# Optimization experiments

Measured on AMD Instinct MI355X. Metric: run time of the kernel, lower is better.

## Reference

```python
import jax, jax.numpy as jnp
import numpy as np

MAX_BLUR = 20.0
MIN_BLUR = 0.5
MIN_SCALE = 0.001


def _dct_matrix(N, dtype):
    """Orthonormal DCT-II matrix C: dct(v) = C @ v (matches torch_dct norm='ortho')."""
    n = jnp.arange(N, dtype=dtype)
    k = n[:, None]
    C = jnp.cos(jnp.pi * (n[None, :] + 0.5) * k / N)
    scale = jnp.where(k == 0, jnp.sqrt(jnp.asarray(1.0 / N, dtype)), jnp.sqrt(jnp.asarray(2.0 / N, dtype)))
    return C * scale


def setup_inputs() -> dict:
    key = jax.random.key(0)
    k1, k2 = jax.random.split(key)
    x = jax.random.normal(k1, (128, 3, 256, 256), dtype=jnp.float32)
    t = jax.random.uniform(k2, (128,), dtype=jnp.float32)
    return {"x": x, "t": t}


def reference(x, t):
    dtype = x.dtype
    N = x.shape[-1]
    # frequency grid: pi * linspace(0, N-1, N) / N, squared and summed over 2D
    freqs = jnp.pi * jnp.arange(N, dtype=dtype) / N
    freq_sq = freqs[:, None] ** 2 + freqs[None, :] ** 2  # [N, N]

    # blur schedule: exp(log(min_blur)*(1-t) + log(max_blur)*t)
    sigmas = jnp.exp(np.log(MIN_BLUR) * (1.0 - t) + np.log(MAX_BLUR) * t)
    sigmas = sigmas[:, None, None, None]  # [B,1,1,1]
    tau = sigmas ** 2 / 2

    fade_freq = jnp.exp(-freq_sq * tau)  # [B,1,N,N]
    fade_freq = jnp.where(fade_freq < 0.01, jnp.zeros((), dtype), fade_freq)

    C = _dct_matrix(N, dtype)  # [N, N]
    # separable 2D DCT-II (ortho): out[k,n] = sum_{h,w} C[k,h] C[n,w] x[h,w]
    dct_x = jnp.einsum('kh,nw,bchw->bckn', C, C, x)
    blurred_dct = dct_x * (fade_freq * (1.0 - MIN_SCALE) + MIN_SCALE)
    # inverse 2D DCT (ortho): transpose matrices
    blurred_x = jnp.einsum('kh,nw,bckn->bchw', C, C, blurred_dct)
    return blurred_x.astype(dtype)
```

## Files before the change

### kernel.cpp

```cpp
#include <hip/hip_runtime.h>
#include <hip/hip_fp16.h>

typedef _Float16 f16;
typedef _Float16 f16x8 __attribute__((ext_vector_type(8)));
typedef _Float16 f16x4 __attribute__((ext_vector_type(4)));
typedef float f32x16 __attribute__((ext_vector_type(16)));

#define NSZ 256
#define NIMG 384

__device__ __forceinline__ int sw(int r, int c) {
  return r * NSZ + (c ^ ((r & 15) << 3));
}

__device__ __forceinline__ int frag_off(int r, int c) {
  return (((((r >> 5) * 16 + (c >> 4)) << 6) + (((c >> 3) & 1) << 5) + (r & 31)) << 3) + (c & 7);
}

__global__ void prep_kernel(f16* __restrict__ Cf, f16* __restrict__ CTf,
                            float* __restrict__ g, const float* __restrict__ t) {
  int k = blockIdx.x;
  int h = threadIdx.x;
  double scale = (k == 0) ? 0.0625 : 0.08838834764831844;
  double val = cos(3.14159265358979323846 * ((double)h + 0.5) * (double)k / 256.0) * scale;
  f16 vh = (f16)((float)val);
  Cf[frag_off(k, h)] = vh;
  CTf[frag_off(h, k)] = vh;
  if (k < 128) {
    float tb = t[k];
    float sg = expf(-0.69314718055994531f * (1.0f - tb) + 2.99573227355399099f * tb);
    float tau = 0.5f * sg * sg;
    float f = 3.14159265358979f * (float)h / 256.0f;
    g[k * NSZ + h] = expf(-f * f * tau);
  }
}

#define TBL_FRAG(Tf, tile, q, lane) (*(const f16x8*)&(Tf)[((((tile) * 16 + (q)) << 6) + (lane)) << 3])

__device__ __forceinline__ void gemm_AL_BT(const f16* L, const f16* __restrict__ Tf,
                                           int rbase, int tB0, int lane,
                                           f32x16 (&acc)[4][2]) {
  int l31 = lane & 31, kh = (lane >> 5) * 8;
#pragma unroll 4
  for (int q = 0; q < 16; ++q) {
    f16x8 a[4], b[2];
#pragma unroll
    for (int fi = 0; fi < 4; ++fi)
      a[fi] = *(const f16x8*)&L[sw(rbase + fi * 32 + l31, q * 16 + kh)];
#pragma unroll
    for (int fj = 0; fj < 2; ++fj)
      b[fj] = TBL_FRAG(Tf, tB0 + fj, q, lane);
#pragma unroll
    for (int fi = 0; fi < 4; ++fi)
#pragma unroll
      for (int fj = 0; fj < 2; ++fj)
        acc[fi][fj] = __builtin_amdgcn_mfma_f32_32x32x16_f16(a[fi], b[fj], acc[fi][fj], 0, 0, 0);
  }
}

__device__ __forceinline__ void writeT(f16* L, int rbase, int cbase, int lane,
                                       const f32x16 (&acc)[4][2]) {
  int l31 = lane & 31, hi4 = (lane >> 5) * 4;
#pragma unroll
  for (int fi = 0; fi < 4; ++fi)
#pragma unroll
    for (int fj = 0; fj < 2; ++fj) {
      int crow = cbase + fj * 32 + l31;
#pragma unroll
      for (int v2 = 0; v2 < 4; ++v2) {
        int colbase = rbase + fi * 32 + v2 * 8 + hi4;
        f16x4 hv;
        hv[0] = (f16)acc[fi][fj][v2 * 4 + 0];
        hv[1] = (f16)acc[fi][fj][v2 * 4 + 1];
        hv[2] = (f16)acc[fi][fj][v2 * 4 + 2];
        hv[3] = (f16)acc[fi][fj][v2 * 4 + 3];
        *(f16x4*)&L[sw(crow, colbase)] = hv;
      }
    }
}

__global__ __launch_bounds__(512, 2) void fused_kernel(
    const float* __restrict__ x, float* __restrict__ out,
    const f16* __restrict__ Cf, const f16* __restrict__ CTf,
    const float* __restrict__ g) {
  __shared__ f16 L[NSZ * NSZ];

  const int img = blockIdx.x;
  const int b = img / 3;
  const float* X = x + (size_t)img * 65536;
  float* Y = out + (size_t)img * 65536;

  const int t = threadIdx.x;
  const int lane = t & 63;
  const int wave = t >> 6;
  const int r0 = (wave >> 2) * 128;
  const int c0 = (wave & 3) * 64;
  const int l31 = lane & 31;
  const int kh = (lane >> 5) * 8;
  const int hi4 = (lane >> 5) * 4;
  const int tB0 = c0 >> 5;

  f32x16 acc[4][2];
  const f32x16 zz = {0.f, 0.f, 0.f, 0.f, 0.f, 0.f, 0.f, 0.f,
                     0.f, 0.f, 0.f, 0.f, 0.f, 0.f, 0.f, 0.f};
#pragma unroll
  for (int fi = 0; fi < 4; ++fi)
#pragma unroll
    for (int fj = 0; fj < 2; ++fj) acc[fi][fj] = zz;

  const int xr_row = t >> 1;
  const int xr_half = (t & 1) * 32;
  float4 xa[2][8];
#pragma unroll
  for (int s = 0; s < 8; ++s) xa[0][s] = *(const float4*)&X[xr_row * NSZ + xr_half + s * 4];

#pragma unroll
  for (int cw = 0; cw < 4; ++cw) {
    int cb = cw & 1;
    if (cw < 3) {
#pragma unroll
      for (int s = 0; s < 8; ++s)
        xa[cb ^ 1][s] = *(const float4*)&X[xr_row * NSZ + (cw + 1) * 64 + xr_half + s * 4];
    }
#pragma unroll
    for (int g8 = 0; g8 < 4; ++g8) {
      float4 a0 = xa[cb][g8 * 2], a1 = xa[cb][g8 * 2 + 1];
      f16x8 v;
      v[0] = (f16)a0.x; v[1] = (f16)a0.y; v[2] = (f16)a0.z; v[3] = (f16)a0.w;
      v[4] = (f16)a1.x; v[5] = (f16)a1.y; v[6] = (f16)a1.z; v[7] = (f16)a1.w;
      *(f16x8*)&L[sw(xr_row, cw * 64 + xr_half + g8 * 8)] = v;
    }
    __syncthreads();
#pragma unroll
    for (int q4 = 0; q4 < 4; ++q4) {
      int q = cw * 4 + q4;
      f16x8 a[4], bfr[2];
#pragma unroll
      for (int fi = 0; fi < 4; ++fi)
        a[fi] = *(const f16x8*)&L[sw(r0 + fi * 32 + l31, q * 16 + kh)];
#pragma unroll
      for (int fj = 0; fj < 2; ++fj)
        bfr[fj] = TBL_FRAG(Cf, tB0 + fj, q, lane);
#pragma unroll
      for (int fi = 0; fi < 4; ++fi)
#pragma unroll
        for (int fj = 0; fj < 2; ++fj)
          acc[fi][fj] = __builtin_amdgcn_mfma_f32_32x32x16_f16(a[fi], bfr[fj], acc[fi][fj], 0, 0, 0);
    }
    __syncthreads();
  }
  writeT(L, r0, c0, lane, acc);
  __syncthreads();

#pragma unroll
  for (int fi = 0; fi < 4; ++fi)
#pragma unroll
    for (int fj = 0; fj < 2; ++fj) acc[fi][fj] = zz;
  gemm_AL_BT(L, Cf, r0, tB0, lane, acc);
  {
    const float* gb = g + b * NSZ;
#pragma unroll
    for (int fj = 0; fj < 2; ++fj) {
      float gk = gb[c0 + fj * 32 + l31];
#pragma unroll
      for (int fi = 0; fi < 4; ++fi) {
#pragma unroll
        for (int v2 = 0; v2 < 4; ++v2) {
          float4 gn = *(const float4*)&gb[r0 + fi * 32 + v2 * 8 + hi4];
          float gnv[4] = {gn.x, gn.y, gn.z, gn.w};
#pragma unroll
          for (int e = 0; e < 4; ++e) {
            float fade = gk * gnv[e];
            float s = ((fade < 0.01f) ? 0.f : fade) * 0.999f + 0.001f;
            acc[fi][fj][v2 * 4 + e] *= s;
          }
        }
      }
    }
  }
  __syncthreads();
  writeT(L, r0, c0, lane, acc);
  __syncthreads();

#pragma unroll
  for (int fi = 0; fi < 4; ++fi)
#pragma unroll
    for (int fj = 0; fj < 2; ++fj) acc[fi][fj] = zz;
  gemm_AL_BT(L, CTf, r0, tB0, lane, acc);
  __syncthreads();
  writeT(L, r0, c0, lane, acc);
  __syncthreads();

#pragma unroll
  for (int fi = 0; fi < 4; ++fi)
#pragma unroll
    for (int fj = 0; fj < 2; ++fj) acc[fi][fj] = zz;
  {
    int tA0 = r0 >> 5;
#pragma unroll 4
    for (int q = 0; q < 16; ++q) {
      f16x8 a[4], bfr[2];
#pragma unroll
      for (int fi = 0; fi < 4; ++fi)
        a[fi] = TBL_FRAG(CTf, tA0 + fi, q, lane);
#pragma unroll
      for (int fj = 0; fj < 2; ++fj)
        bfr[fj] = *(const f16x8*)&L[sw(c0 + fj * 32 + l31, q * 16 + kh)];
#pragma unroll
      for (int fi = 0; fi < 4; ++fi)
#pragma unroll
        for (int fj = 0; fj < 2; ++fj)
          acc[fi][fj] = __builtin_amdgcn_mfma_f32_32x32x16_f16(a[fi], bfr[fj], acc[fi][fj], 0, 0, 0);
    }
  }
#pragma unroll
  for (int fi = 0; fi < 4; ++fi)
#pragma unroll
    for (int fj = 0; fj < 2; ++fj) {
      int w = c0 + fj * 32 + l31;
#pragma unroll
      for (int v2 = 0; v2 < 4; ++v2) {
#pragma unroll
        for (int e = 0; e < 4; ++e) {
          int h = r0 + fi * 32 + v2 * 8 + hi4 + e;
          Y[h * NSZ + w] = acc[fi][fj][v2 * 4 + e];
        }
      }
    }
}

extern "C" void kernel_launch(void* const* d_in, const int* in_sizes, int n_in,
                              void* d_out, int out_size, void* d_ws, size_t ws_size,
                              hipStream_t stream) {
  const float* x = (const float*)d_in[0];
  const float* t = (const float*)d_in[1];
  float* out = (float*)d_out;

  char* ws = (char*)d_ws;
  float* g = (float*)ws;
  f16* Cf = (f16*)(ws + 131072);
  f16* CTf = (f16*)(ws + 262144);

  prep_kernel<<<256, 256, 0, stream>>>(Cf, CTf, g, t);
  fused_kernel<<<NIMG, 512, 0, stream>>>(x, out, Cf, CTf, g);
}
```

Measured before the change: 99.39 us.

## Split fused DCT blur into two half-image kernels with fp16 intermediate in global

Replaces the single per-image fused kernel (512 threads, 128KB LDS) with two kernels that each handle half an image. The first streams 32-row strips of x, does the row and column DCT, applies the fade and writes an fp16 fragment-layout spectrum to workspace. The second runs the inverse DCT on that spectrum. Both use smaller LDS and twice as many blocks, with a block-index swizzle. This is meant to raise occupancy and parallelism, at the cost of an extra global round-trip of fp16 data and one more kernel launch.

```diff
diff --git a/kernel.cpp b/kernel.cpp
--- a/kernel.cpp
+++ b/kernel.cpp
@@ -9,9 +9,8 @@
 #define NSZ 256
 #define NIMG 384
 
-__device__ __forceinline__ int sw(int r, int c) {
-  return r * NSZ + (c ^ ((r & 15) << 3));
-}
+__device__ __forceinline__ int sw(int r, int c) { return r * NSZ + (c ^ ((r & 15) << 3)); }
+__device__ __forceinline__ int sw32(int r, int c) { return r * 32 + (c ^ ((r & 3) << 3)); }
 
 __device__ __forceinline__ int frag_off(int r, int c) {
   return (((((r >> 5) * 16 + (c >> 4)) << 6) + (((c >> 3) & 1) << 5) + (r & 31)) << 3) + (c & 7);
@@ -37,195 +36,192 @@
 
 #define TBL_FRAG(Tf, tile, q, lane) (*(const f16x8*)&(Tf)[((((tile) * 16 + (q)) << 6) + (lane)) << 3])
 
-__device__ __forceinline__ void gemm_AL_BT(const f16* L, const f16* __restrict__ Tf,
-                                           int rbase, int tB0, int lane,
-                                           f32x16 (&acc)[4][2]) {
-  int l31 = lane & 31, kh = (lane >> 5) * 8;
-#pragma unroll 4
-  for (int q = 0; q < 16; ++q) {
-    f16x8 a[4], b[2];
-#pragma unroll
-    for (int fi = 0; fi < 4; ++fi)
-      a[fi] = *(const f16x8*)&L[sw(rbase + fi * 32 + l31, q * 16 + kh)];
-#pragma unroll
-    for (int fj = 0; fj < 2; ++fj)
-      b[fj] = TBL_FRAG(Tf, tB0 + fj, q, lane);
-#pragma unroll
-    for (int fi = 0; fi < 4; ++fi)
-#pragma unroll
-      for (int fj = 0; fj < 2; ++fj)
-        acc[fi][fj] = __builtin_amdgcn_mfma_f32_32x32x16_f16(a[fi], b[fj], acc[fi][fj], 0, 0, 0);
-  }
-}
-
-__device__ __forceinline__ void writeT(f16* L, int rbase, int cbase, int lane,
-                                       const f32x16 (&acc)[4][2]) {
-  int l31 = lane & 31, hi4 = (lane >> 5) * 4;
-#pragma unroll
-  for (int fi = 0; fi < 4; ++fi)
-#pragma unroll
-    for (int fj = 0; fj < 2; ++fj) {
-      int crow = cbase + fj * 32 + l31;
-#pragma unroll
-      for (int v2 = 0; v2 < 4; ++v2) {
-        int colbase = rbase + fi * 32 + v2 * 8 + hi4;
-        f16x4 hv;
-        hv[0] = (f16)acc[fi][fj][v2 * 4 + 0];
-        hv[1] = (f16)acc[fi][fj][v2 * 4 + 1];
-        hv[2] = (f16)acc[fi][fj][v2 * 4 + 2];
-        hv[3] = (f16)acc[fi][fj][v2 * 4 + 3];
-        *(f16x4*)&L[sw(crow, colbase)] = hv;
-      }
-    }
-}
-
-__global__ __launch_bounds__(512, 2) void fused_kernel(
-    const float* __restrict__ x, float* __restrict__ out,
-    const f16* __restrict__ Cf, const f16* __restrict__ CTf,
-    const float* __restrict__ g) {
-  __shared__ f16 L[NSZ * NSZ];
-
-  const int img = blockIdx.x;
-  const int b = img / 3;
+__global__ __launch_bounds__(256, 2) void kernelA(
+    const float* __restrict__ x, f16* __restrict__ Ep,
+    const f16* __restrict__ Cf, const float* __restrict__ g) {
+  __shared__ f16 Xs[32 * NSZ];
+  __shared__ f16 St[128 * 32];
+
+  int bid = blockIdx.x;
+  int wg = (bid & 7) * 96 + (bid >> 3);
+  int img = wg >> 1, half = wg & 1;
+  int b = img / 3;
   const float* X = x + (size_t)img * 65536;
-  float* Y = out + (size_t)img * 65536;
-
-  const int t = threadIdx.x;
-  const int lane = t & 63;
-  const int wave = t >> 6;
-  const int r0 = (wave >> 2) * 128;
-  const int c0 = (wave & 3) * 64;
-  const int l31 = lane & 31;
-  const int kh = (lane >> 5) * 8;
-  const int hi4 = (lane >> 5) * 4;
-  const int tB0 = c0 >> 5;
-
-  f32x16 acc[4][2];
+  f16* Ef = Ep + (size_t)img * 65536;
+
+  int t = threadIdx.x, lane = t & 63, wave = t >> 6;
+  int l31 = lane & 31, hi = lane >> 5;
+  int kh = hi * 8, hi4 = hi * 4;
+
   const f32x16 zz = {0.f, 0.f, 0.f, 0.f, 0.f, 0.f, 0.f, 0.f,
                      0.f, 0.f, 0.f, 0.f, 0.f, 0.f, 0.f, 0.f};
-#pragma unroll
-  for (int fi = 0; fi < 4; ++fi)
-#pragma unroll
-    for (int fj = 0; fj < 2; ++fj) acc[fi][fj] = zz;
-
-  const int xr_row = t >> 1;
-  const int xr_half = (t & 1) * 32;
-  float4 xa[2][8];
-#pragma unroll
-  for (int s = 0; s < 8; ++s) xa[0][s] = *(const float4*)&X[xr_row * NSZ + xr_half + s * 4];
-
-#pragma unroll
-  for (int cw = 0; cw < 4; ++cw) {
-    int cb = cw & 1;
-    if (cw < 3) {
-#pragma unroll
-      for (int s = 0; s < 8; ++s)
-        xa[cb ^ 1][s] = *(const float4*)&X[xr_row * NSZ + (cw + 1) * 64 + xr_half + s * 4];
-    }
-#pragma unroll
-    for (int g8 = 0; g8 < 4; ++g8) {
-      float4 a0 = xa[cb][g8 * 2], a1 = xa[cb][g8 * 2 + 1];
+  f32x16 acc2[8];
+#pragma unroll
+  for (int kt = 0; kt < 8; ++kt) acc2[kt] = zz;
+
+  float4 xr0[8], xr1[8];
+#pragma unroll
+  for (int c = 0; c < 4; ++c) {
+    int gid = t + (c << 8);
+    int r = gid >> 5, gc = (gid & 31) << 3;
+    xr0[c * 2] = *(const float4*)&X[r * NSZ + gc];
+    xr0[c * 2 + 1] = *(const float4*)&X[r * NSZ + gc + 4];
+  }
+
+  for (int hc = 0; hc < 8; ++hc) {
+#pragma unroll
+    for (int c = 0; c < 4; ++c) {
+      int gid = t + (c << 8);
+      int r = gid >> 5, gc = (gid & 31) << 3;
+      float4 a0 = xr0[c * 2], a1 = xr0[c * 2 + 1];
       f16x8 v;
       v[0] = (f16)a0.x; v[1] = (f16)a0.y; v[2] = (f16)a0.z; v[3] = (f16)a0.w;
       v[4] = (f16)a1.x; v[5] = (f16)a1.y; v[6] = (f16)a1.z; v[7] = (f16)a1.w;
-      *(f16x8*)&L[sw(xr_row, cw * 64 + xr_half + g8 * 8)] = v;
+      *(f16x8*)&Xs[sw(r, gc)] = v;
+    }
+    if (hc < 7) {
+#pragma unroll
+      for (int c = 0; c < 4; ++c) {
+        int gid = t + (c << 8);
+        int r = gid >> 5, gc = (gid & 31) << 3;
+        xr1[c * 2] = *(const float4*)&X[((hc + 1) * 32 + r) * NSZ + gc];
+        xr1[c * 2 + 1] = *(const float4*)&X[((hc + 1) * 32 + r) * NSZ + gc + 4];
+      }
     }
     __syncthreads();
-#pragma unroll
-    for (int q4 = 0; q4 < 4; ++q4) {
-      int q = cw * 4 + q4;
-      f16x8 a[4], bfr[2];
-#pragma unroll
-      for (int fi = 0; fi < 4; ++fi)
-        a[fi] = *(const f16x8*)&L[sw(r0 + fi * 32 + l31, q * 16 + kh)];
-#pragma unroll
-      for (int fj = 0; fj < 2; ++fj)
-        bfr[fj] = TBL_FRAG(Cf, tB0 + fj, q, lane);
-#pragma unroll
-      for (int fi = 0; fi < 4; ++fi)
-#pragma unroll
-        for (int fj = 0; fj < 2; ++fj)
-          acc[fi][fj] = __builtin_amdgcn_mfma_f32_32x32x16_f16(a[fi], bfr[fj], acc[fi][fj], 0, 0, 0);
+    f32x16 acc1 = zz;
+#pragma unroll
+    for (int q = 0; q < 16; ++q) {
+      f16x8 a = *(const f16x8*)&Xs[sw(l31, q * 16 + kh)];
+      f16x8 bf = TBL_FRAG(Cf, 4 * half + wave, q, lane);
+      acc1 = __builtin_amdgcn_mfma_f32_32x32x16_f16(a, bf, acc1, 0, 0, 0);
+    }
+#pragma unroll
+    for (int v2 = 0; v2 < 4; ++v2) {
+      f16x4 hv;
+      hv[0] = (f16)acc1[v2 * 4 + 0]; hv[1] = (f16)acc1[v2 * 4 + 1];
+      hv[2] = (f16)acc1[v2 * 4 + 2]; hv[3] = (f16)acc1[v2 * 4 + 3];
+      *(f16x4*)&St[sw32(32 * wave + l31, v2 * 8 + hi4)] = hv;
     }
     __syncthreads();
-  }
-  writeT(L, r0, c0, lane, acc);
+#pragma unroll
+    for (int q = 0; q < 2; ++q) {
+      f16x8 a = *(const f16x8*)&St[sw32(32 * wave + l31, q * 16 + kh)];
+#pragma unroll
+      for (int kt = 0; kt < 8; ++kt) {
+        f16x8 bf = TBL_FRAG(Cf, kt, 2 * hc + q, lane);
+        acc2[kt] = __builtin_amdgcn_mfma_f32_32x32x16_f16(a, bf, acc2[kt], 0, 0, 0);
+      }
+    }
+    if (hc < 7) {
+#pragma unroll
+      for (int s = 0; s < 8; ++s) xr0[s] = xr1[s];
+    }
+  }
+
+  const float* gb = g + b * NSZ;
+#pragma unroll
+  for (int kt = 0; kt < 8; ++kt) {
+    float gk = gb[kt * 32 + l31];
+#pragma unroll
+    for (int v2 = 0; v2 < 4; ++v2) {
+      int nl = 32 * wave + v2 * 8 + hi4;
+      float4 gn4 = *(const float4*)&gb[128 * half + nl];
+      float gnv[4] = {gn4.x, gn4.y, gn4.z, gn4.w};
+      f16x4 hv;
+#pragma unroll
+      for (int e = 0; e < 4; ++e) {
+        float fade = gk * gnv[e];
+        float s = ((fade < 0.01f) ? 0.f : fade) * 0.999f + 0.001f;
+        hv[e] = (f16)(acc2[kt][v2 * 4 + e] * s);
+      }
+      int qg = 2 * wave + (v2 >> 1) + 8 * half;
+      int L = (v2 & 1) * 32 + l31;
+      *(f16x4*)&Ef[((((kt * 16 + qg) << 6) + L) << 3) + hi4] = hv;
+    }
+  }
+}
+
+__global__ __launch_bounds__(256, 2) void kernelB(
+    const f16* __restrict__ Ep, float* __restrict__ out, const f16* __restrict__ CTf) {
+  __shared__ f16 G[128 * NSZ];
+
+  int bid = blockIdx.x;
+  int wg = (bid & 7) * 96 + (bid >> 3);
+  int img = wg >> 1, half = wg & 1;
+  const f16* Ef = Ep + (size_t)img * 65536;
+  float* Y = out + (size_t)img * 65536 + 128 * half;
+
+  int t = threadIdx.x, lane = t & 63, wave = t >> 6;
+  int l31 = lane & 31, hi = lane >> 5, kh = hi * 8, hi4 = hi * 4;
+
+  const f32x16 zz = {0.f, 0.f, 0.f, 0.f, 0.f, 0.f, 0.f, 0.f,
+                     0.f, 0.f, 0.f, 0.f, 0.f, 0.f, 0.f, 0.f};
+  f32x16 acc[2][4];
+#pragma unroll
+  for (int fi = 0; fi < 2; ++fi)
+#pragma unroll
+    for (int fj = 0; fj < 4; ++fj) acc[fi][fj] = zz;
+
+#pragma unroll 4
+  for (int q = 0; q < 16; ++q) {
+    f16x8 a[2], bf[4];
+    a[0] = TBL_FRAG(Ef, wave * 2 + 0, q, lane);
+    a[1] = TBL_FRAG(Ef, wave * 2 + 1, q, lane);
+#pragma unroll
+    for (int fj = 0; fj < 4; ++fj) bf[fj] = TBL_FRAG(CTf, 4 * half + fj, q, lane);
+#pragma unroll
+    for (int fi = 0; fi < 2; ++fi)
+#pragma unroll
+      for (int fj = 0; fj < 4; ++fj)
+        acc[fi][fj] = __builtin_amdgcn_mfma_f32_32x32x16_f16(a[fi], bf[fj], acc[fi][fj], 0, 0, 0);
+  }
+#pragma unroll
+  for (int fi = 0; fi < 2; ++fi)
+#pragma unroll
+    for (int fj = 0; fj < 4; ++fj) {
+      int crow = fj * 32 + l31;
+#pragma unroll
+      for (int v2 = 0; v2 < 4; ++v2) {
+        int colbase = (wave * 2 + fi) * 32 + v2 * 8 + hi4;
+        f16x4 hv;
+        hv[0] = (f16)acc[fi][fj][v2 * 4 + 0]; hv[1] = (f16)acc[fi][fj][v2 * 4 + 1];
+        hv[2] = (f16)acc[fi][fj][v2 * 4 + 2]; hv[3] = (f16)acc[fi][fj][v2 * 4 + 3];
+        *(f16x4*)&G[sw(crow, colbase)] = hv;
+      }
+    }
   __syncthreads();
 
 #pragma unroll
-  for (int fi = 0; fi < 4; ++fi)
-#pragma unroll
-    for (int fj = 0; fj < 2; ++fj) acc[fi][fj] = zz;
-  gemm_AL_BT(L, Cf, r0, tB0, lane, acc);
-  {
-    const float* gb = g + b * NSZ;
-#pragma unroll
-    for (int fj = 0; fj < 2; ++fj) {
-      float gk = gb[c0 + fj * 32 + l31];
-#pragma unroll
-      for (int fi = 0; fi < 4; ++fi) {
-#pragma unroll
-        for (int v2 = 0; v2 < 4; ++v2) {
-          float4 gn = *(const float4*)&gb[r0 + fi * 32 + v2 * 8 + hi4];
-          float gnv[4] = {gn.x, gn.y, gn.z, gn.w};
-#pragma unroll
-          for (int e = 0; e < 4; ++e) {
-            float fade = gk * gnv[e];
-            float s = ((fade < 0.01f) ? 0.f : fade) * 0.999f + 0.001f;
-            acc[fi][fj][v2 * 4 + e] *= s;
-          }
-        }
-      }
-    }
-  }
-  __syncthreads();
-  writeT(L, r0, c0, lane, acc);
-  __syncthreads();
-
-#pragma unroll
-  for (int fi = 0; fi < 4; ++fi)
-#pragma unroll
-    for (int fj = 0; fj < 2; ++fj) acc[fi][fj] = zz;
-  gemm_AL_BT(L, CTf, r0, tB0, lane, acc);
-  __syncthreads();
-  writeT(L, r0, c0, lane, acc);
-  __syncthreads();
-
-#pragma unroll
-  for (int fi = 0; fi < 4; ++fi)
-#pragma unroll
-    for (int fj = 0; fj < 2; ++fj) acc[fi][fj] = zz;
-  {
-    int tA0 = r0 >> 5;
+  for (int fi = 0; fi < 2; ++fi)
+#pragma unroll
+    for (int fj = 0; fj < 4; ++fj) acc[fi][fj] = zz;
 #pragma unroll 4
-    for (int q = 0; q < 16; ++q) {
-      f16x8 a[4], bfr[2];
-#pragma unroll
-      for (int fi = 0; fi < 4; ++fi)
-        a[fi] = TBL_FRAG(CTf, tA0 + fi, q, lane);
-#pragma unroll
-      for (int fj = 0; fj < 2; ++fj)
-        bfr[fj] = *(const f16x8*)&L[sw(c0 + fj * 32 + l31, q * 16 + kh)];
-#pragma unroll
-      for (int fi = 0; fi < 4; ++fi)
-#pragma unroll
-        for (int fj = 0; fj < 2; ++fj)
-          acc[fi][fj] = __builtin_amdgcn_mfma_f32_32x32x16_f16(a[fi], bfr[fj], acc[fi][fj], 0, 0, 0);
-    }
-  }
-#pragma unroll
-  for (int fi = 0; fi < 4; ++fi)
-#pragma unroll
-    for (int fj = 0; fj < 2; ++fj) {
-      int w = c0 + fj * 32 + l31;
-#pragma unroll
-      for (int v2 = 0; v2 < 4; ++v2) {
+  for (int q = 0; q < 16; ++q) {
+    f16x8 a[2], bf[4];
+    a[0] = TBL_FRAG(CTf, wave * 2 + 0, q, lane);
+    a[1] = TBL_FRAG(CTf, wave * 2 + 1, q, lane);
+#pragma unroll
+    for (int fj = 0; fj < 4; ++fj)
+      bf[fj] = *(const f16x8*)&G[sw(fj * 32 + l31, q * 16 + kh)];
+#pragma unroll
+    for (int fi = 0; fi < 2; ++fi)
+#pragma unroll
+      for (int fj = 0; fj < 4; ++fj)
+        acc[fi][fj] = __builtin_amdgcn_mfma_f32_32x32x16_f16(a[fi], bf[fj], acc[fi][fj], 0, 0, 0);
+  }
+#pragma unroll
+  for (int fi = 0; fi < 2; ++fi)
+#pragma unroll
+    for (int fj = 0; fj < 4; ++fj) {
+      int w = fj * 32 + l31;
+#pragma unroll
+      for (int v2 = 0; v2 < 4; ++v2)
 #pragma unroll
         for (int e = 0; e < 4; ++e) {
-          int h = r0 + fi * 32 + v2 * 8 + hi4 + e;
+          int h = (wave * 2 + fi) * 32 + v2 * 8 + hi4 + e;
           Y[h * NSZ + w] = acc[fi][fj][v2 * 4 + e];
         }
-      }
     }
 }
 
@@ -240,7 +236,9 @@
   float* g = (float*)ws;
   f16* Cf = (f16*)(ws + 131072);
   f16* CTf = (f16*)(ws + 262144);
+  f16* Ep = (f16*)(ws + 393216);
 
   prep_kernel<<<256, 256, 0, stream>>>(Cf, CTf, g, t);
-  fused_kernel<<<NIMG, 512, 0, stream>>>(x, out, Cf, CTf, g);
-}
+  kernelA<<<NIMG * 2, 256, 0, stream>>>(x, Ep, Cf, g);
+  kernelB<<<NIMG * 2, 256, 0, stream>>>(Ep, out, CTf);
+}
```

Measured after the change: 173.1 us. 74.2% more time.

## Truncate DCT frequency band per batch and add residual identity term

Applied to the files above, without the earlier changes.

Computes per-batch how many low frequencies survive the fade threshold, then skips every MFMA tile whose frequency index lies beyond that cutoff across the forward and inverse DCT passes. The constant MIN_SCALE term is moved out of the spectral multiplier and added back exactly as 0.001*x in the output, since the inverse DCT of a scaled identity is that identity. The x prefetch is also restructured from double buffering to a single buffer to save registers. The cutoff uses a slightly looser threshold (0.0099) on the 1D gain to stay conservative, and the speedup depends on the t-distribution giving small cutoffs.

```diff
diff --git a/kernel.cpp b/kernel.cpp
--- a/kernel.cpp
+++ b/kernel.cpp
@@ -9,16 +9,15 @@
 #define NSZ 256
 #define NIMG 384
 
-__device__ __forceinline__ int sw(int r, int c) {
-  return r * NSZ + (c ^ ((r & 15) << 3));
-}
+__device__ __forceinline__ int sw(int r, int c) { return r * NSZ + (c ^ ((r & 15) << 3)); }
 
 __device__ __forceinline__ int frag_off(int r, int c) {
   return (((((r >> 5) * 16 + (c >> 4)) << 6) + (((c >> 3) & 1) << 5) + (r & 31)) << 3) + (c & 7);
 }
 
 __global__ void prep_kernel(f16* __restrict__ Cf, f16* __restrict__ CTf,
-                            float* __restrict__ g, const float* __restrict__ t) {
+                            float* __restrict__ g, int* __restrict__ Kq,
+                            const float* __restrict__ t) {
   int k = blockIdx.x;
   int h = threadIdx.x;
   double scale = (k == 0) ? 0.0625 : 0.08838834764831844;
@@ -26,45 +25,36 @@
   f16 vh = (f16)((float)val);
   Cf[frag_off(k, h)] = vh;
   CTf[frag_off(h, k)] = vh;
+  int pred = 0;
   if (k < 128) {
     float tb = t[k];
     float sg = expf(-0.69314718055994531f * (1.0f - tb) + 2.99573227355399099f * tb);
     float tau = 0.5f * sg * sg;
     float f = 3.14159265358979f * (float)h / 256.0f;
-    g[k * NSZ + h] = expf(-f * f * tau);
+    float gv = expf(-f * f * tau);
+    g[k * NSZ + h] = gv;
+    pred = (gv >= 0.0099f) ? 1 : 0;
+  }
+  int cnt = __syncthreads_count(pred);
+  if (k < 128 && h == 0) {
+    int K = ((cnt + 31) >> 5) << 5;
+    if (K < 32) K = 32;
+    if (K > 256) K = 256;
+    Kq[k] = K;
   }
 }
 
 #define TBL_FRAG(Tf, tile, q, lane) (*(const f16x8*)&(Tf)[((((tile) * 16 + (q)) << 6) + (lane)) << 3])
 
-__device__ __forceinline__ void gemm_AL_BT(const f16* L, const f16* __restrict__ Tf,
-                                           int rbase, int tB0, int lane,
-                                           f32x16 (&acc)[4][2]) {
-  int l31 = lane & 31, kh = (lane >> 5) * 8;
-#pragma unroll 4
-  for (int q = 0; q < 16; ++q) {
-    f16x8 a[4], b[2];
-#pragma unroll
-    for (int fi = 0; fi < 4; ++fi)
-      a[fi] = *(const f16x8*)&L[sw(rbase + fi * 32 + l31, q * 16 + kh)];
-#pragma unroll
-    for (int fj = 0; fj < 2; ++fj)
-      b[fj] = TBL_FRAG(Tf, tB0 + fj, q, lane);
-#pragma unroll
-    for (int fi = 0; fi < 4; ++fi)
-#pragma unroll
-      for (int fj = 0; fj < 2; ++fj)
-        acc[fi][fj] = __builtin_amdgcn_mfma_f32_32x32x16_f16(a[fi], b[fj], acc[fi][fj], 0, 0, 0);
-  }
-}
-
 __device__ __forceinline__ void writeT(f16* L, int rbase, int cbase, int lane,
-                                       const f32x16 (&acc)[4][2]) {
+                                       const f32x16 (&acc)[4][2], int rowLim, int colLim) {
   int l31 = lane & 31, hi4 = (lane >> 5) * 4;
 #pragma unroll
-  for (int fi = 0; fi < 4; ++fi)
+  for (int fi = 0; fi < 4; ++fi) {
+    if (rbase + fi * 32 >= rowLim) continue;
 #pragma unroll
     for (int fj = 0; fj < 2; ++fj) {
+      if (cbase + fj * 32 >= colLim) continue;
       int crow = cbase + fj * 32 + l31;
 #pragma unroll
       for (int v2 = 0; v2 < 4; ++v2) {
@@ -77,16 +67,19 @@
         *(f16x4*)&L[sw(crow, colbase)] = hv;
       }
     }
+  }
 }
 
 __global__ __launch_bounds__(512, 2) void fused_kernel(
     const float* __restrict__ x, float* __restrict__ out,
     const f16* __restrict__ Cf, const f16* __restrict__ CTf,
-    const float* __restrict__ g) {
+    const float* __restrict__ g, const int* __restrict__ KqA) {
   __shared__ f16 L[NSZ * NSZ];
 
   const int img = blockIdx.x;
   const int b = img / 3;
+  const int Kq = KqA[b];
+  const int nq = Kq >> 4;
   const float* X = x + (size_t)img * 65536;
   float* Y = out + (size_t)img * 65536;
 
@@ -99,79 +92,103 @@
   const int kh = (lane >> 5) * 8;
   const int hi4 = (lane >> 5) * 4;
   const int tB0 = c0 >> 5;
-
-  f32x16 acc[4][2];
+  const int tA0 = r0 >> 5;
+  const bool actB0 = tB0 * 32 < Kq;
+  const bool actB1 = (tB0 + 1) * 32 < Kq;
+
   const f32x16 zz = {0.f, 0.f, 0.f, 0.f, 0.f, 0.f, 0.f, 0.f,
                      0.f, 0.f, 0.f, 0.f, 0.f, 0.f, 0.f, 0.f};
-#pragma unroll
-  for (int fi = 0; fi < 4; ++fi)
-#pragma unroll
-    for (int fj = 0; fj < 2; ++fj) acc[fi][fj] = zz;
+  f32x16 acc[4][2];
+#pragma unroll
+  for (int fi = 0; fi < 4; ++fi) { acc[fi][0] = zz; acc[fi][1] = zz; }
 
   const int xr_row = t >> 1;
   const int xr_half = (t & 1) * 32;
-  float4 xa[2][8];
-#pragma unroll
-  for (int s = 0; s < 8; ++s) xa[0][s] = *(const float4*)&X[xr_row * NSZ + xr_half + s * 4];
-
-#pragma unroll
+  float4 xa[8];
+#pragma unroll
+  for (int s = 0; s < 8; ++s) xa[s] = *(const float4*)&X[xr_row * NSZ + xr_half + s * 4];
+
   for (int cw = 0; cw < 4; ++cw) {
-    int cb = cw & 1;
-    if (cw < 3) {
-#pragma unroll
-      for (int s = 0; s < 8; ++s)
-        xa[cb ^ 1][s] = *(const float4*)&X[xr_row * NSZ + (cw + 1) * 64 + xr_half + s * 4];
-    }
 #pragma unroll
     for (int g8 = 0; g8 < 4; ++g8) {
-      float4 a0 = xa[cb][g8 * 2], a1 = xa[cb][g8 * 2 + 1];
+      float4 a0 = xa[g8 * 2], a1 = xa[g8 * 2 + 1];
       f16x8 v;
       v[0] = (f16)a0.x; v[1] = (f16)a0.y; v[2] = (f16)a0.z; v[3] = (f16)a0.w;
       v[4] = (f16)a1.x; v[5] = (f16)a1.y; v[6] = (f16)a1.z; v[7] = (f16)a1.w;
       *(f16x8*)&L[sw(xr_row, cw * 64 + xr_half + g8 * 8)] = v;
     }
     __syncthreads();
+    if (cw < 3) {
+#pragma unroll
+      for (int s = 0; s < 8; ++s)
+        xa[s] = *(const float4*)&X[xr_row * NSZ + (cw + 1) * 64 + xr_half + s * 4];
+    }
 #pragma unroll
     for (int q4 = 0; q4 < 4; ++q4) {
       int q = cw * 4 + q4;
-      f16x8 a[4], bfr[2];
+      f16x8 a[4];
 #pragma unroll
       for (int fi = 0; fi < 4; ++fi)
         a[fi] = *(const f16x8*)&L[sw(r0 + fi * 32 + l31, q * 16 + kh)];
-#pragma unroll
-      for (int fj = 0; fj < 2; ++fj)
-        bfr[fj] = TBL_FRAG(Cf, tB0 + fj, q, lane);
-#pragma unroll
-      for (int fi = 0; fi < 4; ++fi)
-#pragma unroll
-        for (int fj = 0; fj < 2; ++fj)
-          acc[fi][fj] = __builtin_amdgcn_mfma_f32_32x32x16_f16(a[fi], bfr[fj], acc[fi][fj], 0, 0, 0);
-    }
-    __syncthreads();
-  }
-  writeT(L, r0, c0, lane, acc);
-  __syncthreads();
-
-#pragma unroll
-  for (int fi = 0; fi < 4; ++fi)
-#pragma unroll
-    for (int fj = 0; fj < 2; ++fj) acc[fi][fj] = zz;
-  gemm_AL_BT(L, Cf, r0, tB0, lane, acc);
-  {
+      if (actB0) {
+        f16x8 bf = TBL_FRAG(Cf, tB0, q, lane);
+#pragma unroll
+        for (int fi = 0; fi < 4; ++fi)
+          acc[fi][0] = __builtin_amdgcn_mfma_f32_32x32x16_f16(a[fi], bf, acc[fi][0], 0, 0, 0);
+      }
+      if (actB1) {
+        f16x8 bf = TBL_FRAG(Cf, tB0 + 1, q, lane);
+#pragma unroll
+        for (int fi = 0; fi < 4; ++fi)
+          acc[fi][1] = __builtin_amdgcn_mfma_f32_32x32x16_f16(a[fi], bf, acc[fi][1], 0, 0, 0);
+      }
+    }
+  }
+  __syncthreads();
+  writeT(L, r0, c0, lane, acc, 256, Kq);
+  __syncthreads();
+
+  if (r0 < Kq) {
+#pragma unroll
+    for (int fi = 0; fi < 4; ++fi) { acc[fi][0] = zz; acc[fi][1] = zz; }
+#pragma unroll 4
+    for (int q = 0; q < 16; ++q) {
+      f16x8 a[4];
+#pragma unroll
+      for (int fi = 0; fi < 4; ++fi)
+        if (r0 + fi * 32 < Kq)
+          a[fi] = *(const f16x8*)&L[sw(r0 + fi * 32 + l31, q * 16 + kh)];
+      if (actB0) {
+        f16x8 bf = TBL_FRAG(Cf, tB0, q, lane);
+#pragma unroll
+        for (int fi = 0; fi < 4; ++fi)
+          if (r0 + fi * 32 < Kq)
+            acc[fi][0] = __builtin_amdgcn_mfma_f32_32x32x16_f16(a[fi], bf, acc[fi][0], 0, 0, 0);
+      }
+      if (actB1) {
+        f16x8 bf = TBL_FRAG(Cf, tB0 + 1, q, lane);
+#pragma unroll
+        for (int fi = 0; fi < 4; ++fi)
+          if (r0 + fi * 32 < Kq)
+            acc[fi][1] = __builtin_amdgcn_mfma_f32_32x32x16_f16(a[fi], bf, acc[fi][1], 0, 0, 0);
+      }
+    }
     const float* gb = g + b * NSZ;
 #pragma unroll
     for (int fj = 0; fj < 2; ++fj) {
+      if ((tB0 + fj) * 32 >= Kq) continue;
       float gk = gb[c0 + fj * 32 + l31];
 #pragma unroll
       for (int fi = 0; fi < 4; ++fi) {
+        if (r0 + fi * 32 >= Kq) continue;
 #pragma unroll
         for (int v2 = 0; v2 < 4; ++v2) {
-          float4 gn = *(const float4*)&gb[r0 + fi * 32 + v2 * 8 + hi4];
-          float gnv[4] = {gn.x, gn.y, gn.z, gn.w};
+          float4 gn4 = *(const float4*)&gb[r0 + fi * 32 + v2 * 8 + hi4];
+          float gnv[4] = {gn4.x, gn4.y, gn4.z, gn4.w};
 #pragma unroll
           for (int e = 0; e < 4; ++e) {
             float fade = gk * gnv[e];
-            float s = ((fade < 0.01f) ? 0.f : fade) * 0.999f + 0.001f;
+            float s = (fade < 0.01f) ? 0.f : 0.999f * fade;
             acc[fi][fj][v2 * 4 + e] *= s;
           }
         }
@@ -179,54 +196,55 @@
     }
   }
   __syncthreads();
-  writeT(L, r0, c0, lane, acc);
-  __syncthreads();
-
-#pragma unroll
-  for (int fi = 0; fi < 4; ++fi)
-#pragma unroll
-    for (int fj = 0; fj < 2; ++fj) acc[fi][fj] = zz;
-  gemm_AL_BT(L, CTf, r0, tB0, lane, acc);
-  __syncthreads();
-  writeT(L, r0, c0, lane, acc);
-  __syncthreads();
-
-#pragma unroll
-  for (int fi = 0; fi < 4; ++fi)
-#pragma unroll
-    for (int fj = 0; fj < 2; ++fj) acc[fi][fj] = zz;
-  {
-    int tA0 = r0 >> 5;
-#pragma unroll 4
-    for (int q = 0; q < 16; ++q) {
-      f16x8 a[4], bfr[2];
-#pragma unroll
-      for (int fi = 0; fi < 4; ++fi)
-        a[fi] = TBL_FRAG(CTf, tA0 + fi, q, lane);
-#pragma unroll
-      for (int fj = 0; fj < 2; ++fj)
-        bfr[fj] = *(const f16x8*)&L[sw(c0 + fj * 32 + l31, q * 16 + kh)];
-#pragma unroll
-      for (int fi = 0; fi < 4; ++fi)
-#pragma unroll
-        for (int fj = 0; fj < 2; ++fj)
-          acc[fi][fj] = __builtin_amdgcn_mfma_f32_32x32x16_f16(a[fi], bfr[fj], acc[fi][fj], 0, 0, 0);
-    }
-  }
-#pragma unroll
-  for (int fi = 0; fi < 4; ++fi)
-#pragma unroll
-    for (int fj = 0; fj < 2; ++fj) {
-      int w = c0 + fj * 32 + l31;
-#pragma unroll
-      for (int v2 = 0; v2 < 4; ++v2) {
+  writeT(L, r0, c0, lane, acc, Kq, Kq);
+  __syncthreads();
+
+#pragma unroll
+  for (int fi = 0; fi < 4; ++fi) { acc[fi][0] = zz; acc[fi][1] = zz; }
+  if (r0 < Kq) {
+    for (int q = 0; q < nq; ++q) {
+      f16x8 a[4];
+#pragma unroll
+      for (int fi = 0; fi < 4; ++fi)
+        if (r0 + fi * 32 < Kq)
+          a[fi] = *(const f16x8*)&L[sw(r0 + fi * 32 + l31, q * 16 + kh)];
+      f16x8 b0 = TBL_FRAG(CTf, tB0, q, lane);
+      f16x8 b1 = TBL_FRAG(CTf, tB0 + 1, q, lane);
+#pragma unroll
+      for (int fi = 0; fi < 4; ++fi)
+        if (r0 + fi * 32 < Kq) {
+          acc[fi][0] = __builtin_amdgcn_mfma_f32_32x32x16_f16(a[fi], b0, acc[fi][0], 0, 0, 0);
+          acc[fi][1] = __builtin_amdgcn_mfma_f32_32x32x16_f16(a[fi], b1, acc[fi][1], 0, 0, 0);
+        }
+    }
+  }
+  __syncthreads();
+  writeT(L, r0, c0, lane, acc, Kq, 256);
+  __syncthreads();
+
+#pragma unroll
+  for (int fj = 0; fj < 2; ++fj) {
+#pragma unroll
+    for (int fi = 0; fi < 4; ++fi) acc[fi][fj] = zz;
+    for (int q = 0; q < nq; ++q) {
+      f16x8 bf = *(const f16x8*)&L[sw(c0 + fj * 32 + l31, q * 16 + kh)];
+#pragma unroll
+      for (int fi = 0; fi < 4; ++fi) {
+        f16x8 a = TBL_FRAG(CTf, tA0 + fi, q, lane);
+        acc[fi][fj] = __builtin_amdgcn_mfma_f32_32x32x16_f16(a, bf, acc[fi][fj], 0, 0, 0);
+      }
+    }
+    int w = c0 + fj * 32 + l31;
+#pragma unroll
+    for (int fi = 0; fi < 4; ++fi)
+#pragma unroll
+      for (int v2 = 0; v2 < 4; ++v2)
 #pragma unroll
         for (int e = 0; e < 4; ++e) {
           int h = r0 + fi * 32 + v2 * 8 + hi4 + e;
-          Y[h * NSZ + w] = acc[fi][fj][v2 * 4 + e];
+          Y[h * NSZ + w] = acc[fi][fj][v2 * 4 + e] + 0.001f * X[h * NSZ + w];
         }
-      }
-    }
+  }
 }
 
 extern "C" void kernel_launch(void* const* d_in, const int* in_sizes, int n_in,
@@ -240,7 +258,8 @@
   float* g = (float*)ws;
   f16* Cf = (f16*)(ws + 131072);
   f16* CTf = (f16*)(ws + 262144);
-
-  prep_kernel<<<256, 256, 0, stream>>>(Cf, CTf, g, t);
-  fused_kernel<<<NIMG, 512, 0, stream>>>(x, out, Cf, CTf, g);
-}
+  int* Kq = (int*)(ws + 393216);
+
+  prep_kernel<<<256, 256, 0, stream>>>(Cf, CTf, g, Kq, t);
+  fused_kernel<<<NIMG, 512, 0, stream>>>(x, out, Cf, CTf, g, Kq);
+}
```

Result: slower. 117.4 us (+18.1%).
